# Kernel tuning notes

Measured on AMD Instinct MI355X. Metric: run time of the kernel, lower is better.

The kernel has to match this reference:

```python
import jax, jax.numpy as jnp
import numpy as np

NHEAD = 8
HEAD_DIM = 64
HIDDEN = 512
ROPE_BASE = 10000.0


def _rope_cos_sin(L, dim, dtype):
    inv_freq = 1.0 / (ROPE_BASE ** (jnp.arange(0, dim, 2, dtype=jnp.float32) / dim))
    t = jnp.arange(L, dtype=jnp.float32)
    freqs = jnp.outer(t, inv_freq)                # [L, dim/2]
    emb = jnp.concatenate([freqs, freqs], axis=-1)  # [L, dim]
    return jnp.cos(emb).astype(dtype), jnp.sin(emb).astype(dtype)


def _rotate_half(x):
    x1, x2 = jnp.split(x, 2, axis=-1)
    return jnp.concatenate([-x2, x1], axis=-1)


def setup_inputs() -> dict:
    key = jax.random.key(0)
    ks = jax.random.split(key, 5)
    B, L = 8, 1024
    scale = 0.02
    return {
        "x": jax.random.normal(ks[0], (B, L, HIDDEN), dtype=jnp.float32),
        "Wq": jax.random.normal(ks[1], (HIDDEN, HIDDEN), dtype=jnp.float32) * scale,
        "Wk": jax.random.normal(ks[2], (HIDDEN, HIDDEN), dtype=jnp.float32) * scale,
        "Wv": jax.random.normal(ks[3], (HIDDEN, HIDDEN), dtype=jnp.float32) * scale,
        "Wo": jax.random.normal(ks[4], (HIDDEN, HIDDEN), dtype=jnp.float32) * scale,
    }


def reference(x, Wq, Wk, Wv, Wo):
    B, L, _ = x.shape
    # QKV projections (nn.Linear stores weight as [out, in]; y = x @ W.T)
    def proj(W):
        y = jnp.einsum('bld,ed->ble', x, W)
        return y.reshape(B, L, NHEAD, HEAD_DIM).transpose(0, 2, 1, 3)  # [B,H,L,Dh]
    q, k, v = proj(Wq), proj(Wk), proj(Wv)

    cos, sin = _rope_cos_sin(L, HEAD_DIM, x.dtype)   # [L, Dh]
    cos = cos[None, None]                            # [1,1,L,Dh]
    sin = sin[None, None]
    q = q * cos + _rotate_half(q) * sin
    k = k * cos + _rotate_half(k) * sin

    # scaled dot-product attention (no mask, eval mode -> dropout 0)
    scores = jnp.einsum('bhqd,bhkd->bhqk', q, k) / jnp.sqrt(jnp.asarray(HEAD_DIM, x.dtype))
    attn = jax.nn.softmax(scores, axis=-1)
    out = jnp.einsum('bhqk,bhkd->bhqd', attn, v)     # [B,H,L,Dh]
    out = out.transpose(0, 2, 1, 3).reshape(B, L, HIDDEN)
    return jnp.einsum('ble,oe->blo', out, Wo)
```

## Files before the change

kernel.cpp:

```cpp
#include <hip/hip_runtime.h>
#include <math.h>


#define BB 8
#define LL 1024
#define HH 8
#define DH 64
#define HID 512

typedef __bf16 bf16x8 __attribute__((ext_vector_type(8)));
typedef float f32x4 __attribute__((ext_vector_type(4)));
typedef float f32x16 __attribute__((ext_vector_type(16)));
typedef unsigned short u16x8 __attribute__((ext_vector_type(8)));
typedef unsigned short u16x4 __attribute__((ext_vector_type(4)));
typedef unsigned u32x4 __attribute__((ext_vector_type(4)));

__device__ inline unsigned short f2bf(float f) {
    union { float f; unsigned u; } v; v.f = f;
    unsigned r = v.u + 0x7fffu + ((v.u >> 16) & 1u);
    return (unsigned short)(r >> 16);
}

#define GLOAD_LDS16(g, l) __builtin_amdgcn_global_load_lds( \
    (const __attribute__((address_space(1))) unsigned int*)(g), \
    (__attribute__((address_space(3))) unsigned int*)(l), 16, 0, 0)

__device__ inline bf16x8 pack8(float e0, float e1, float e2, float e3,
                               float e4, float e5, float e6, float e7) {
    unsigned a0, a1, a2, a3;
    asm("v_cvt_pk_bf16_f32 %0, %1, %2" : "=v"(a0) : "v"(e0), "v"(e1));
    asm("v_cvt_pk_bf16_f32 %0, %1, %2" : "=v"(a1) : "v"(e2), "v"(e3));
    asm("v_cvt_pk_bf16_f32 %0, %1, %2" : "=v"(a2) : "v"(e4), "v"(e5));
    asm("v_cvt_pk_bf16_f32 %0, %1, %2" : "=v"(a3) : "v"(e6), "v"(e7));
    asm("v_permlane32_swap_b32 %0, %1" : "+v"(a0), "+v"(a2));
    asm("v_permlane32_swap_b32 %0, %1" : "+v"(a1), "+v"(a3));
    u32x4 wv; wv[0] = a0; wv[1] = a1; wv[2] = a2; wv[3] = a3;
    return *(bf16x8*)&wv;
}

#define Z16 {0.f,0.f,0.f,0.f,0.f,0.f,0.f,0.f,0.f,0.f,0.f,0.f,0.f,0.f,0.f,0.f}

__global__ __launch_bounds__(256) void convert_kernel(
    const float* __restrict__ x, const float* __restrict__ Wq,
    const float* __restrict__ Wk, const float* __restrict__ Wv,
    const float* __restrict__ Wo,
    unsigned short* __restrict__ xb, unsigned short* __restrict__ wqb,
    unsigned short* __restrict__ wkb, unsigned short* __restrict__ wvb,
    unsigned short* __restrict__ wob,
    float* __restrict__ cos_t, float* __restrict__ sin_t)
{
    int blk = blockIdx.x;
    if (blk >= 2560) {
        int idx = (blk - 2560) * 256 + threadIdx.x;
        int l = idx >> 5, j = idx & 31;
        float inv = exp2f(-(float)j * (13.287712379549449f / 32.0f));
        float th = (float)l * inv;
        cos_t[idx] = cosf(th);
        sin_t[idx] = sinf(th);
        return;
    }
    const float* s; unsigned short* d; int off;
    if (blk < 2048) { s = x; d = xb; off = blk; }
    else {
        int t = (blk - 2048) >> 7;
        off = (blk - 2048) & 127;
        s = (t == 0) ? Wq : (t == 1) ? Wk : (t == 2) ? Wv : Wo;
        d = (t == 0) ? wqb : (t == 1) ? wkb : (t == 2) ? wvb : wob;
    }
    size_t base = ((size_t)off * 256 + threadIdx.x) * 8;
    float4 a = *(const float4*)(s + base);
    float4 b = *(const float4*)(s + base + 4);
    u16x8 pk;
    pk[0] = f2bf(a.x); pk[1] = f2bf(a.y); pk[2] = f2bf(a.z); pk[3] = f2bf(a.w);
    pk[4] = f2bf(b.x); pk[5] = f2bf(b.y); pk[6] = f2bf(b.z); pk[7] = f2bf(b.w);
    *(u16x8*)(d + base) = pk;
}

__global__ __launch_bounds__(256) void qkv_gemm_kernel(
    const unsigned short* __restrict__ xb, const unsigned short* __restrict__ Wqb,
    const unsigned short* __restrict__ Wkb, const unsigned short* __restrict__ Wvb,
    const float* __restrict__ cos_t, const float* __restrict__ sin_t,
    unsigned short* __restrict__ Qb, unsigned short* __restrict__ Kb,
    unsigned short* __restrict__ Vt)
{
    __shared__ unsigned short As[128 * 32];
    __shared__ unsigned short Bs[128 * 32];

    const int mt = blockIdx.x;
    const int nt = blockIdx.y;
    const int mbase = mt * 128;
    const int mat = nt >> 2;
    const unsigned short* W = (mat == 0) ? Wqb : ((mat == 1) ? Wkb : Wvb);
    const int nW = (nt & 3) * 128;

    const int tid = threadIdx.x;
    const int w = tid >> 6, lane = tid & 63;
    const int wr = w >> 1, wc = w & 1;
    const int l15 = lane & 15, koff = (lane >> 4) * 8;
    const int srow = (lane >> 2);
    const int scol = (lane & 3) * 8;

    f32x4 acc[4][4];
    #pragma unroll
    for (int i = 0; i < 4; ++i)
        #pragma unroll
        for (int j = 0; j < 4; ++j) acc[i][j] = (f32x4){0.f, 0.f, 0.f, 0.f};

    for (int kc = 0; kc < 512; kc += 32) {
        __syncthreads();
        #pragma unroll
        for (int j = 0; j < 2; ++j) {
            int row = w * 32 + j * 16;
            GLOAD_LDS16(xb + (size_t)(mbase + row + srow) * 512 + kc + scol,
                        As + row * 32);
            GLOAD_LDS16(W + (size_t)(nW + row + srow) * 512 + kc + scol,
                        Bs + row * 32);
        }
        __syncthreads();

        bf16x8 af[4], bf[4];
        #pragma unroll
        for (int mi = 0; mi < 4; ++mi)
            af[mi] = *(const bf16x8*)&As[(wr * 64 + mi * 16 + l15) * 32 + koff];
        #pragma unroll
        for (int ni = 0; ni < 4; ++ni)
            bf[ni] = *(const bf16x8*)&Bs[(wc * 64 + ni * 16 + l15) * 32 + koff];
        #pragma unroll
        for (int mi = 0; mi < 4; ++mi)
            #pragma unroll
            for (int ni = 0; ni < 4; ++ni)
                acc[mi][ni] = __builtin_amdgcn_mfma_f32_16x16x32_bf16(
                    af[mi], bf[ni], acc[mi][ni], 0, 0, 0);
    }

    const int h = (nt & 3) * 2 + wc;
    if (mat < 2) {
        unsigned short* D = (mat == 0) ? Qb : Kb;
        const float sc = (mat == 0) ? 0.18033688011112042f  : 1.0f;
        #pragma unroll
        for (int mi = 0; mi < 4; ++mi) {
            int m = mbase + wr * 64 + mi * 16 + (lane >> 4) * 4;
            int b = m >> 10, l0 = m & 1023;
            #pragma unroll
            for (int r = 0; r < 4; ++r) {
                int l = l0 + r;
                float c0 = cos_t[l * 32 + l15],      s0 = sin_t[l * 32 + l15];
                float c1 = cos_t[l * 32 + 16 + l15], s1 = sin_t[l * 32 + 16 + l15];
                float a0 = acc[mi][0][r], a1 = acc[mi][1][r];
                float a2 = acc[mi][2][r], a3 = acc[mi][3][r];
                float o0 = (a0 * c0 - a2 * s0) * sc;
                float o1 = (a1 * c1 - a3 * s1) * sc;
                float o2 = (a2 * c0 + a0 * s0) * sc;
                float o3 = (a3 * c1 + a1 * s1) * sc;
                size_t rowbase = ((size_t)(b * HH + h) * LL + l) * 64;
                D[rowbase +  0 + l15] = f2bf(o0);
                D[rowbase + 16 + l15] = f2bf(o1);
                D[rowbase + 32 + l15] = f2bf(o2);
                D[rowbase + 48 + l15] = f2bf(o3);
            }
        }
    } else {
        #pragma unroll
        for (int mi = 0; mi < 4; ++mi) {
            int m = mbase + wr * 64 + mi * 16 + (lane >> 4) * 4;
            int b = m >> 10, l0 = m & 1023;
            #pragma unroll
            for (int ni = 0; ni < 4; ++ni) {
                int d = ni * 16 + l15;
                u16x4 pk;
                #pragma unroll
                for (int r = 0; r < 4; ++r) pk[r] = f2bf(acc[mi][ni][r]);
                *(u16x4*)(Vt + ((size_t)(b * HH + h) * 64 + d) * LL + l0) = pk;
            }
        }
    }
}

__global__ __launch_bounds__(256) void attn_kernel(
    const unsigned short* __restrict__ Q, const unsigned short* __restrict__ K,
    const unsigned short* __restrict__ Vt, unsigned short* __restrict__ O)
{
    __shared__ unsigned short Ks[2][64 * 64];
    __shared__ unsigned short Vs[2][64 * 64];

    const int wgid = blockIdx.x;
    const int xcd = wgid & 7;
    const int j = wgid >> 3;
    const int bh = xcd * 8 + (j >> 3);
    const int qt = j & 7;
    const int b = bh >> 3, h = bh & 7;
    const int tid = threadIdx.x;
    const int w = tid >> 6;
    const int lane = tid & 63;
    const int l31 = lane & 31;
    const int hi5 = lane >> 5;

    const unsigned short* Qp = Q + (size_t)bh * LL * 64;
    const unsigned short* Kp = K + (size_t)bh * LL * 64;
    const unsigned short* Vp = Vt + (size_t)bh * 64 * LL;

    const int sr0 = w * 8 + (lane >> 3);
    const int sr1 = 32 + w * 8 + (lane >> 3);
    const int scsw = ((lane & 7) * 8) ^ (((lane >> 3) & 7) * 8);
    const int sd0 = w * 512;
    const int sd1 = 2048 + w * 512;

    const int q0 = qt * 128 + w * 32;

    bf16x8 qf0 = *(const bf16x8*)(Qp + (size_t)(q0 + l31) * 64 +  0 + hi5 * 8);
    bf16x8 qf1 = *(const bf16x8*)(Qp + (size_t)(q0 + l31) * 64 + 16 + hi5 * 8);
    bf16x8 qf2 = *(const bf16x8*)(Qp + (size_t)(q0 + l31) * 64 + 32 + hi5 * 8);
    bf16x8 qf3 = *(const bf16x8*)(Qp + (size_t)(q0 + l31) * 64 + 48 + hi5 * 8);

    const int swz = (l31 & 7) * 8;
    const int co0 = ( 0 + hi5 * 8) ^ swz;
    const int co1 = (16 + hi5 * 8) ^ swz;
    const int co2 = (32 + hi5 * 8) ^ swz;
    const int co3 = (48 + hi5 * 8) ^ swz;
    const int rA = l31 * 64;
    const int rB = (32 + l31) * 64;

    float lsum = 0.f;
    f32x16 opv0 = Z16, opv1 = Z16;

    GLOAD_LDS16(Kp + (size_t)sr0 * 64 + scsw, &Ks[0][sd0]);
    GLOAD_LDS16(Kp + (size_t)sr1 * 64 + scsw, &Ks[0][sd1]);
    GLOAD_LDS16(Vp + (size_t)sr0 * LL + scsw, &Vs[0][sd0]);
    GLOAD_LDS16(Vp + (size_t)sr1 * LL + scsw, &Vs[0][sd1]);
    __syncthreads();

    for (int kt = 0; kt < 16; ++kt) {
        const int cur = kt & 1, nxt = cur ^ 1;
        const int kbase = kt * 64;

        if (kt < 15) {
            GLOAD_LDS16(Kp + (size_t)(kbase + 64 + sr0) * 64 + scsw, &Ks[nxt][sd0]);
            GLOAD_LDS16(Kp + (size_t)(kbase + 64 + sr1) * 64 + scsw, &Ks[nxt][sd1]);
            GLOAD_LDS16(Vp + (size_t)sr0 * LL + kbase + 64 + scsw, &Vs[nxt][sd0]);
            GLOAD_LDS16(Vp + (size_t)sr1 * LL + kbase + 64 + scsw, &Vs[nxt][sd1]);
        }

        f32x16 s0 = Z16, s1 = Z16;
        __builtin_amdgcn_s_setprio(1);
        {
            bf16x8 kA, kB;
            kA = *(const bf16x8*)&Ks[cur][rA + co0];
            kB = *(const bf16x8*)&Ks[cur][rB + co0];
            s0 = __builtin_amdgcn_mfma_f32_32x32x16_bf16(kA, qf0, s0, 0, 0, 0);
            s1 = __builtin_amdgcn_mfma_f32_32x32x16_bf16(kB, qf0, s1, 0, 0, 0);
            kA = *(const bf16x8*)&Ks[cur][rA + co1];
            kB = *(const bf16x8*)&Ks[cur][rB + co1];
            s0 = __builtin_amdgcn_mfma_f32_32x32x16_bf16(kA, qf1, s0, 0, 0, 0);
            s1 = __builtin_amdgcn_mfma_f32_32x32x16_bf16(kB, qf1, s1, 0, 0, 0);
            kA = *(const bf16x8*)&Ks[cur][rA + co2];
            kB = *(const bf16x8*)&Ks[cur][rB + co2];
            s0 = __builtin_amdgcn_mfma_f32_32x32x16_bf16(kA, qf2, s0, 0, 0, 0);
            s1 = __builtin_amdgcn_mfma_f32_32x32x16_bf16(kB, qf2, s1, 0, 0, 0);
            kA = *(const bf16x8*)&Ks[cur][rA + co3];
            kB = *(const bf16x8*)&Ks[cur][rB + co3];
            s0 = __builtin_amdgcn_mfma_f32_32x32x16_bf16(kA, qf3, s0, 0, 0, 0);
            s1 = __builtin_amdgcn_mfma_f32_32x32x16_bf16(kB, qf3, s1, 0, 0, 0);
        }
        __builtin_amdgcn_s_setprio(0);

        float e[16], f[16];
        #pragma unroll
        for (int i = 0; i < 16; ++i) e[i] = exp2f(s0[i]);
        #pragma unroll
        for (int i = 0; i < 16; ++i) f[i] = exp2f(s1[i]);
        lsum += (((e[0]+e[1])+(e[2]+e[3])) + ((e[4]+e[5])+(e[6]+e[7])))
              + (((e[8]+e[9])+(e[10]+e[11])) + ((e[12]+e[13])+(e[14]+e[15])));
        lsum += (((f[0]+f[1])+(f[2]+f[3])) + ((f[4]+f[5])+(f[6]+f[7])))
              + (((f[8]+f[9])+(f[10]+f[11])) + ((f[12]+f[13])+(f[14]+f[15])));
        bf16x8 pf0 = pack8(e[0], e[1], e[2], e[3], e[4], e[5], e[6], e[7]);
        bf16x8 pf1 = pack8(e[8], e[9], e[10], e[11], e[12], e[13], e[14], e[15]);
        bf16x8 pf2 = pack8(f[0], f[1], f[2], f[3], f[4], f[5], f[6], f[7]);
        bf16x8 pf3 = pack8(f[8], f[9], f[10], f[11], f[12], f[13], f[14], f[15]);

        __builtin_amdgcn_s_setprio(1);
        {
            bf16x8 vA, vB;
            vA = *(const bf16x8*)&Vs[cur][rA + co0];
            vB = *(const bf16x8*)&Vs[cur][rB + co0];
            opv0 = __builtin_amdgcn_mfma_f32_32x32x16_bf16(vA, pf0, opv0, 0, 0, 0);
            opv1 = __builtin_amdgcn_mfma_f32_32x32x16_bf16(vB, pf0, opv1, 0, 0, 0);
            vA = *(const bf16x8*)&Vs[cur][rA + co1];
            vB = *(const bf16x8*)&Vs[cur][rB + co1];
            opv0 = __builtin_amdgcn_mfma_f32_32x32x16_bf16(vA, pf1, opv0, 0, 0, 0);
            opv1 = __builtin_amdgcn_mfma_f32_32x32x16_bf16(vB, pf1, opv1, 0, 0, 0);
            vA = *(const bf16x8*)&Vs[cur][rA + co2];
            vB = *(const bf16x8*)&Vs[cur][rB + co2];
            opv0 = __builtin_amdgcn_mfma_f32_32x32x16_bf16(vA, pf2, opv0, 0, 0, 0);
            opv1 = __builtin_amdgcn_mfma_f32_32x32x16_bf16(vB, pf2, opv1, 0, 0, 0);
            vA = *(const bf16x8*)&Vs[cur][rA + co3];
            vB = *(const bf16x8*)&Vs[cur][rB + co3];
            opv0 = __builtin_amdgcn_mfma_f32_32x32x16_bf16(vA, pf3, opv0, 0, 0, 0);
            opv1 = __builtin_amdgcn_mfma_f32_32x32x16_bf16(vB, pf3, opv1, 0, 0, 0);
        }
        __builtin_amdgcn_s_setprio(0);

        __syncthreads();
    }

    lsum += __shfl_xor(lsum, 32);

    const float inv = 1.f / lsum;
    unsigned short* ob = O + (size_t)(b * LL + q0 + l31) * HID + h * 64;
    #pragma unroll
    for (int rg = 0; rg < 4; ++rg) {
        u16x4 pkA, pkB;
        #pragma unroll
        for (int rr = 0; rr < 4; ++rr) {
            pkA[rr] = f2bf(opv0[rg * 4 + rr] * inv);
            pkB[rr] = f2bf(opv1[rg * 4 + rr] * inv);
        }
        *(u16x4*)(ob + rg * 8 + hi5 * 4)      = pkA;
        *(u16x4*)(ob + 32 + rg * 8 + hi5 * 4) = pkB;
    }
}

__global__ __launch_bounds__(256) void out_gemm_kernel(
    const unsigned short* __restrict__ AOb, const unsigned short* __restrict__ Wob,
    float* __restrict__ out)
{
    __shared__ unsigned short As[128 * 32];
    __shared__ unsigned short Bs[64 * 32];

    const int mt = blockIdx.x;
    const int nt = blockIdx.y;
    const int mbase = mt * 128;
    const int nbase = nt * 64;

    const int tid = threadIdx.x;
    const int w = tid >> 6, lane = tid & 63;
    const int wr = w >> 1, wc = w & 1;
    const int l15 = lane & 15, koff = (lane >> 4) * 8;
    const int srow = (lane >> 2);
    const int scol = (lane & 3) * 8;

    f32x4 acc[4][2];
    #pragma unroll
    for (int i = 0; i < 4; ++i)
        #pragma unroll
        for (int j = 0; j < 2; ++j) acc[i][j] = (f32x4){0.f, 0.f, 0.f, 0.f};

    for (int kc = 0; kc < 512; kc += 32) {
        __syncthreads();
        #pragma unroll
        for (int j = 0; j < 2; ++j) {
            int row = w * 32 + j * 16;
            GLOAD_LDS16(AOb + (size_t)(mbase + row + srow) * 512 + kc + scol,
                        As + row * 32);
        }
        {
            int row = w * 16 + srow;
            GLOAD_LDS16(Wob + (size_t)(nbase + row) * 512 + kc + scol,
                        Bs + (w * 16) * 32);
        }
        __syncthreads();

        bf16x8 af[4], bf[2];
        #pragma unroll
        for (int mi = 0; mi < 4; ++mi)
            af[mi] = *(const bf16x8*)&As[(wr * 64 + mi * 16 + l15) * 32 + koff];
        #pragma unroll
        for (int ni = 0; ni < 2; ++ni)
            bf[ni] = *(const bf16x8*)&Bs[(wc * 32 + ni * 16 + l15) * 32 + koff];
        #pragma unroll
        for (int mi = 0; mi < 4; ++mi)
            #pragma unroll
            for (int ni = 0; ni < 2; ++ni)
                acc[mi][ni] = __builtin_amdgcn_mfma_f32_16x16x32_bf16(
                    af[mi], bf[ni], acc[mi][ni], 0, 0, 0);
    }

    #pragma unroll
    for (int mi = 0; mi < 4; ++mi) {
        int m = mbase + wr * 64 + mi * 16 + (lane >> 4) * 4;
        #pragma unroll
        for (int r = 0; r < 4; ++r) {
            size_t rowbase = (size_t)(m + r) * 512 + nbase + wc * 32;
            #pragma unroll
            for (int ni = 0; ni < 2; ++ni)
                out[rowbase + ni * 16 + l15] = acc[mi][ni][r];
        }
    }
}

extern "C" void kernel_launch(void* const* d_in, const int* in_sizes, int n_in,
                              void* d_out, int out_size, void* d_ws, size_t ws_size,
                              hipStream_t stream) {
    const float* x  = (const float*)d_in[0];
    const float* Wq = (const float*)d_in[1];
    const float* Wk = (const float*)d_in[2];
    const float* Wv = (const float*)d_in[3];
    const float* Wo = (const float*)d_in[4];
    float* out = (float*)d_out;

    const size_t tblN = (size_t)LL * 32;
    const size_t qkvN = (size_t)BB * HH * LL * 64;
    const size_t wN   = (size_t)HID * HID;

    float* cos_t = (float*)d_ws;
    float* sin_t = cos_t + tblN;
    unsigned short* Qb  = (unsigned short*)(sin_t + tblN);
    unsigned short* Kb  = Qb + qkvN;
    unsigned short* Vt  = Kb + qkvN;
    unsigned short* xb  = Vt + qkvN;
    unsigned short* Wqb = xb + qkvN;
    unsigned short* Wkb = Wqb + wN;
    unsigned short* Wvb = Wkb + wN;
    unsigned short* Wob = Wvb + wN;
    unsigned short* AOb = Wob + wN;

    hipLaunchKernelGGL(convert_kernel, dim3(2048 + 512 + 128), dim3(256), 0, stream,
                       x, Wq, Wk, Wv, Wo, xb, Wqb, Wkb, Wvb, Wob, cos_t, sin_t);
    hipLaunchKernelGGL(qkv_gemm_kernel, dim3(64, 12), dim3(256), 0, stream,
                       xb, Wqb, Wkb, Wvb, cos_t, sin_t, Qb, Kb, Vt);
    hipLaunchKernelGGL(attn_kernel, dim3(512), dim3(256), 0, stream,
                       Qb, Kb, Vt, AOb);
    hipLaunchKernelGGL(out_gemm_kernel, dim3(64, 8), dim3(256), 0, stream,
                       AOb, Wob, out);
}
```

Measured before the change: 83.64 us.

## Double K-chunk depth in QKV GEMM and attention KV tiles with swizzled LDS

The QKV projection GEMM now stages 64-wide K slices per iteration, with an XOR-swizzled LDS layout to avoid bank conflicts, and issues two MFMAs per tile pair. This halves the number of barrier-synchronised iterations. The attention kernel processes 128 keys per tile instead of 64, so there are half as many barriers and prefetch rounds. This doubles LDS usage per block, which may reduce occupancy, and raises register pressure from more score accumulators and exp values.

```diff
diff --git a/kernel.cpp b/kernel.cpp
--- a/kernel.cpp
+++ b/kernel.cpp
@@ -83,8 +83,8 @@
     unsigned short* __restrict__ Qb, unsigned short* __restrict__ Kb,
     unsigned short* __restrict__ Vt)
 {
-    __shared__ unsigned short As[128 * 32];
-    __shared__ unsigned short Bs[128 * 32];
+    __shared__ unsigned short As[128 * 64];
+    __shared__ unsigned short Bs[128 * 64];
 
     const int mt = blockIdx.x;
     const int nt = blockIdx.y;
@@ -97,8 +97,13 @@
     const int w = tid >> 6, lane = tid & 63;
     const int wr = w >> 1, wc = w & 1;
     const int l15 = lane & 15, koff = (lane >> 4) * 8;
-    const int srow = (lane >> 2);
-    const int scol = (lane & 3) * 8;
+
+    const int srow = w * 8 + (lane >> 3);
+    const int ssw = ((lane & 7) * 8) ^ (((lane >> 3) & 7) * 8);
+
+    const int rsw = (l15 & 7) * 8;
+    const int ck0 = (koff +  0) ^ rsw;
+    const int ck1 = (koff + 32) ^ rsw;
 
     f32x4 acc[4][4];
     #pragma unroll
@@ -106,31 +111,40 @@
         #pragma unroll
         for (int j = 0; j < 4; ++j) acc[i][j] = (f32x4){0.f, 0.f, 0.f, 0.f};
 
-    for (int kc = 0; kc < 512; kc += 32) {
+    for (int kc = 0; kc < 512; kc += 64) {
         __syncthreads();
         #pragma unroll
-        for (int j = 0; j < 2; ++j) {
-            int row = w * 32 + j * 16;
-            GLOAD_LDS16(xb + (size_t)(mbase + row + srow) * 512 + kc + scol,
-                        As + row * 32);
-            GLOAD_LDS16(W + (size_t)(nW + row + srow) * 512 + kc + scol,
-                        Bs + row * 32);
+        for (int j = 0; j < 4; ++j) {
+            int row = j * 32 + srow;
+            GLOAD_LDS16(xb + (size_t)(mbase + row) * 512 + kc + ssw,
+                        As + j * 2048 + w * 512);
+            GLOAD_LDS16(W + (size_t)(nW + row) * 512 + kc + ssw,
+                        Bs + j * 2048 + w * 512);
         }
         __syncthreads();
 
-        bf16x8 af[4], bf[4];
+        bf16x8 af[4][2], bf[4][2];
+        #pragma unroll
+        for (int mi = 0; mi < 4; ++mi) {
+            int r = (wr * 64 + mi * 16 + l15) * 64;
+            af[mi][0] = *(const bf16x8*)&As[r + ck0];
+            af[mi][1] = *(const bf16x8*)&As[r + ck1];
+        }
+        #pragma unroll
+        for (int ni = 0; ni < 4; ++ni) {
+            int r = (wc * 64 + ni * 16 + l15) * 64;
+            bf[ni][0] = *(const bf16x8*)&Bs[r + ck0];
+            bf[ni][1] = *(const bf16x8*)&Bs[r + ck1];
+        }
         #pragma unroll
         for (int mi = 0; mi < 4; ++mi)
-            af[mi] = *(const bf16x8*)&As[(wr * 64 + mi * 16 + l15) * 32 + koff];
-        #pragma unroll
-        for (int ni = 0; ni < 4; ++ni)
-            bf[ni] = *(const bf16x8*)&Bs[(wc * 64 + ni * 16 + l15) * 32 + koff];
-        #pragma unroll
-        for (int mi = 0; mi < 4; ++mi)
-            #pragma unroll
-            for (int ni = 0; ni < 4; ++ni)
+            #pragma unroll
+            for (int ni = 0; ni < 4; ++ni) {
                 acc[mi][ni] = __builtin_amdgcn_mfma_f32_16x16x32_bf16(
-                    af[mi], bf[ni], acc[mi][ni], 0, 0, 0);
+                    af[mi][0], bf[ni][0], acc[mi][ni], 0, 0, 0);
+                acc[mi][ni] = __builtin_amdgcn_mfma_f32_16x16x32_bf16(
+                    af[mi][1], bf[ni][1], acc[mi][ni], 0, 0, 0);
+            }
     }
 
     const int h = (nt & 3) * 2 + wc;
@@ -180,8 +194,8 @@
     const unsigned short* __restrict__ Q, const unsigned short* __restrict__ K,
     const unsigned short* __restrict__ Vt, unsigned short* __restrict__ O)
 {
-    __shared__ unsigned short Ks[2][64 * 64];
-    __shared__ unsigned short Vs[2][64 * 64];
+    __shared__ unsigned short Ks[2][128 * 64];
+    __shared__ unsigned short Vs[2][64 * 128];
 
     const int wgid = blockIdx.x;
     const int xcd = wgid & 7;
@@ -199,11 +213,10 @@
     const unsigned short* Kp = K + (size_t)bh * LL * 64;
     const unsigned short* Vp = Vt + (size_t)bh * 64 * LL;
 
-    const int sr0 = w * 8 + (lane >> 3);
-    const int sr1 = 32 + w * 8 + (lane >> 3);
-    const int scsw = ((lane & 7) * 8) ^ (((lane >> 3) & 7) * 8);
-    const int sd0 = w * 512;
-    const int sd1 = 2048 + w * 512;
+    const int srK = w * 8 + (lane >> 3);
+    const int sswK = ((lane & 7) * 8) ^ (((lane >> 3) & 7) * 8);
+    const int srV = w * 4 + (lane >> 4);
+    const int sswV = ((lane & 15) * 8) ^ ((srV & 7) * 8);
 
     const int q0 = qt * 128 + w * 32;
 
@@ -217,85 +230,136 @@
     const int co1 = (16 + hi5 * 8) ^ swz;
     const int co2 = (32 + hi5 * 8) ^ swz;
     const int co3 = (48 + hi5 * 8) ^ swz;
-    const int rA = l31 * 64;
-    const int rB = (32 + l31) * 64;
+    const int rK = l31 * 64;
+    int cv[8];
+    #pragma unroll
+    for (int ksl = 0; ksl < 8; ++ksl) cv[ksl] = (ksl * 16 + hi5 * 8) ^ swz;
+    const int rVA = l31 * 128;
+    const int rVB = rVA + 32 * 128;
 
     float lsum = 0.f;
     f32x16 opv0 = Z16, opv1 = Z16;
 
-    GLOAD_LDS16(Kp + (size_t)sr0 * 64 + scsw, &Ks[0][sd0]);
-    GLOAD_LDS16(Kp + (size_t)sr1 * 64 + scsw, &Ks[0][sd1]);
-    GLOAD_LDS16(Vp + (size_t)sr0 * LL + scsw, &Vs[0][sd0]);
-    GLOAD_LDS16(Vp + (size_t)sr1 * LL + scsw, &Vs[0][sd1]);
+    #pragma unroll
+    for (int c = 0; c < 4; ++c) {
+        GLOAD_LDS16(Kp + (size_t)(c * 32 + srK) * 64 + sswK, &Ks[0][c * 2048 + w * 512]);
+        GLOAD_LDS16(Vp + (size_t)(c * 16 + srV) * LL + sswV, &Vs[0][c * 2048 + w * 512]);
+    }
     __syncthreads();
 
-    for (int kt = 0; kt < 16; ++kt) {
+    for (int kt = 0; kt < 8; ++kt) {
         const int cur = kt & 1, nxt = cur ^ 1;
-        const int kbase = kt * 64;
-
-        if (kt < 15) {
-            GLOAD_LDS16(Kp + (size_t)(kbase + 64 + sr0) * 64 + scsw, &Ks[nxt][sd0]);
-            GLOAD_LDS16(Kp + (size_t)(kbase + 64 + sr1) * 64 + scsw, &Ks[nxt][sd1]);
-            GLOAD_LDS16(Vp + (size_t)sr0 * LL + kbase + 64 + scsw, &Vs[nxt][sd0]);
-            GLOAD_LDS16(Vp + (size_t)sr1 * LL + kbase + 64 + scsw, &Vs[nxt][sd1]);
-        }
-
-        f32x16 s0 = Z16, s1 = Z16;
+        const int kbase = kt * 128;
+
+        if (kt < 7) {
+            #pragma unroll
+            for (int c = 0; c < 4; ++c) {
+                GLOAD_LDS16(Kp + (size_t)(kbase + 128 + c * 32 + srK) * 64 + sswK,
+                            &Ks[nxt][c * 2048 + w * 512]);
+                GLOAD_LDS16(Vp + (size_t)(c * 16 + srV) * LL + kbase + 128 + sswV,
+                            &Vs[nxt][c * 2048 + w * 512]);
+            }
+        }
+
+        f32x16 s0 = Z16, s1 = Z16, s2 = Z16, s3 = Z16;
         __builtin_amdgcn_s_setprio(1);
         {
-            bf16x8 kA, kB;
-            kA = *(const bf16x8*)&Ks[cur][rA + co0];
-            kB = *(const bf16x8*)&Ks[cur][rB + co0];
+            bf16x8 kA;
+            kA = *(const bf16x8*)&Ks[cur][0 * 2048 + rK + co0];
             s0 = __builtin_amdgcn_mfma_f32_32x32x16_bf16(kA, qf0, s0, 0, 0, 0);
-            s1 = __builtin_amdgcn_mfma_f32_32x32x16_bf16(kB, qf0, s1, 0, 0, 0);
-            kA = *(const bf16x8*)&Ks[cur][rA + co1];
-            kB = *(const bf16x8*)&Ks[cur][rB + co1];
+            kA = *(const bf16x8*)&Ks[cur][0 * 2048 + rK + co1];
             s0 = __builtin_amdgcn_mfma_f32_32x32x16_bf16(kA, qf1, s0, 0, 0, 0);
-            s1 = __builtin_amdgcn_mfma_f32_32x32x16_bf16(kB, qf1, s1, 0, 0, 0);
-            kA = *(const bf16x8*)&Ks[cur][rA + co2];
-            kB = *(const bf16x8*)&Ks[cur][rB + co2];
+            kA = *(const bf16x8*)&Ks[cur][0 * 2048 + rK + co2];
             s0 = __builtin_amdgcn_mfma_f32_32x32x16_bf16(kA, qf2, s0, 0, 0, 0);
-            s1 = __builtin_amdgcn_mfma_f32_32x32x16_bf16(kB, qf2, s1, 0, 0, 0);
-            kA = *(const bf16x8*)&Ks[cur][rA + co3];
-            kB = *(const bf16x8*)&Ks[cur][rB + co3];
+            kA = *(const bf16x8*)&Ks[cur][0 * 2048 + rK + co3];
             s0 = __builtin_amdgcn_mfma_f32_32x32x16_bf16(kA, qf3, s0, 0, 0, 0);
-            s1 = __builtin_amdgcn_mfma_f32_32x32x16_bf16(kB, qf3, s1, 0, 0, 0);
+
+            kA = *(const bf16x8*)&Ks[cur][1 * 2048 + rK + co0];
+            s1 = __builtin_amdgcn_mfma_f32_32x32x16_bf16(kA, qf0, s1, 0, 0, 0);
+            kA = *(const bf16x8*)&Ks[cur][1 * 2048 + rK + co1];
+            s1 = __builtin_amdgcn_mfma_f32_32x32x16_bf16(kA, qf1, s1, 0, 0, 0);
+            kA = *(const bf16x8*)&Ks[cur][1 * 2048 + rK + co2];
+            s1 = __builtin_amdgcn_mfma_f32_32x32x16_bf16(kA, qf2, s1, 0, 0, 0);
+            kA = *(const bf16x8*)&Ks[cur][1 * 2048 + rK + co3];
+            s1 = __builtin_amdgcn_mfma_f32_32x32x16_bf16(kA, qf3, s1, 0, 0, 0);
+
+            kA = *(const bf16x8*)&Ks[cur][2 * 2048 + rK + co0];
+            s2 = __builtin_amdgcn_mfma_f32_32x32x16_bf16(kA, qf0, s2, 0, 0, 0);
+            kA = *(const bf16x8*)&Ks[cur][2 * 2048 + rK + co1];
+            s2 = __builtin_amdgcn_mfma_f32_32x32x16_bf16(kA, qf1, s2, 0, 0, 0);
+            kA = *(const bf16x8*)&Ks[cur][2 * 2048 + rK + co2];
+            s2 = __builtin_amdgcn_mfma_f32_32x32x16_bf16(kA, qf2, s2, 0, 0, 0);
+            kA = *(const bf16x8*)&Ks[cur][2 * 2048 + rK + co3];
+            s2 = __builtin_amdgcn_mfma_f32_32x32x16_bf16(kA, qf3, s2, 0, 0, 0);
+
+            kA = *(const bf16x8*)&Ks[cur][3 * 2048 + rK + co0];
+            s3 = __builtin_amdgcn_mfma_f32_32x32x16_bf16(kA, qf0, s3, 0, 0, 0);
+            kA = *(const bf16x8*)&Ks[cur][3 * 2048 + rK + co1];
+            s3 = __builtin_amdgcn_mfma_f32_32x32x16_bf16(kA, qf1, s3, 0, 0, 0);
+            kA = *(const bf16x8*)&Ks[cur][3 * 2048 + rK + co2];
+            s3 = __builtin_amdgcn_mfma_f32_32x32x16_bf16(kA, qf2, s3, 0, 0, 0);
+            kA = *(const bf16x8*)&Ks[cur][3 * 2048 + rK + co3];
+            s3 = __builtin_amdgcn_mfma_f32_32x32x16_bf16(kA, qf3, s3, 0, 0, 0);
         }
         __builtin_amdgcn_s_setprio(0);
 
-        float e[16], f[16];
-        #pragma unroll
-        for (int i = 0; i < 16; ++i) e[i] = exp2f(s0[i]);
-        #pragma unroll
-        for (int i = 0; i < 16; ++i) f[i] = exp2f(s1[i]);
-        lsum += (((e[0]+e[1])+(e[2]+e[3])) + ((e[4]+e[5])+(e[6]+e[7])))
-              + (((e[8]+e[9])+(e[10]+e[11])) + ((e[12]+e[13])+(e[14]+e[15])));
-        lsum += (((f[0]+f[1])+(f[2]+f[3])) + ((f[4]+f[5])+(f[6]+f[7])))
-              + (((f[8]+f[9])+(f[10]+f[11])) + ((f[12]+f[13])+(f[14]+f[15])));
+        float e[16], f[16], g[16], hh[16];
+        #pragma unroll
+        for (int i = 0; i < 16; ++i) e[i]  = exp2f(s0[i]);
+        #pragma unroll
+        for (int i = 0; i < 16; ++i) f[i]  = exp2f(s1[i]);
+        #pragma unroll
+        for (int i = 0; i < 16; ++i) g[i]  = exp2f(s2[i]);
+        #pragma unroll
+        for (int i = 0; i < 16; ++i) hh[i] = exp2f(s3[i]);
+        #pragma unroll
+        for (int i = 0; i < 16; ++i) lsum += e[i] + f[i];
+        #pragma unroll
+        for (int i = 0; i < 16; ++i) lsum += g[i] + hh[i];
         bf16x8 pf0 = pack8(e[0], e[1], e[2], e[3], e[4], e[5], e[6], e[7]);
         bf16x8 pf1 = pack8(e[8], e[9], e[10], e[11], e[12], e[13], e[14], e[15]);
         bf16x8 pf2 = pack8(f[0], f[1], f[2], f[3], f[4], f[5], f[6], f[7]);
         bf16x8 pf3 = pack8(f[8], f[9], f[10], f[11], f[12], f[13], f[14], f[15]);
+        bf16x8 pf4 = pack8(g[0], g[1], g[2], g[3], g[4], g[5], g[6], g[7]);
+        bf16x8 pf5 = pack8(g[8], g[9], g[10], g[11], g[12], g[13], g[14], g[15]);
+        bf16x8 pf6 = pack8(hh[0], hh[1], hh[2], hh[3], hh[4], hh[5], hh[6], hh[7]);
+        bf16x8 pf7 = pack8(hh[8], hh[9], hh[10], hh[11], hh[12], hh[13], hh[14], hh[15]);
 
         __builtin_amdgcn_s_setprio(1);
         {
             bf16x8 vA, vB;
-            vA = *(const bf16x8*)&Vs[cur][rA + co0];
-            vB = *(const bf16x8*)&Vs[cur][rB + co0];
+            vA = *(const bf16x8*)&Vs[cur][rVA + cv[0]];
+            vB = *(const bf16x8*)&Vs[cur][rVB + cv[0]];
             opv0 = __builtin_amdgcn_mfma_f32_32x32x16_bf16(vA, pf0, opv0, 0, 0, 0);
             opv1 = __builtin_amdgcn_mfma_f32_32x32x16_bf16(vB, pf0, opv1, 0, 0, 0);
-            vA = *(const bf16x8*)&Vs[cur][rA + co1];
-            vB = *(const bf16x8*)&Vs[cur][rB + co1];
+            vA = *(const bf16x8*)&Vs[cur][rVA + cv[1]];
+            vB = *(const bf16x8*)&Vs[cur][rVB + cv[1]];
             opv0 = __builtin_amdgcn_mfma_f32_32x32x16_bf16(vA, pf1, opv0, 0, 0, 0);
             opv1 = __builtin_amdgcn_mfma_f32_32x32x16_bf16(vB, pf1, opv1, 0, 0, 0);
-            vA = *(const bf16x8*)&Vs[cur][rA + co2];
-            vB = *(const bf16x8*)&Vs[cur][rB + co2];
+            vA = *(const bf16x8*)&Vs[cur][rVA + cv[2]];
+            vB = *(const bf16x8*)&Vs[cur][rVB + cv[2]];
             opv0 = __builtin_amdgcn_mfma_f32_32x32x16_bf16(vA, pf2, opv0, 0, 0, 0);
             opv1 = __builtin_amdgcn_mfma_f32_32x32x16_bf16(vB, pf2, opv1, 0, 0, 0);
-            vA = *(const bf16x8*)&Vs[cur][rA + co3];
-            vB = *(const bf16x8*)&Vs[cur][rB + co3];
+            vA = *(const bf16x8*)&Vs[cur][rVA + cv[3]];
+            vB = *(const bf16x8*)&Vs[cur][rVB + cv[3]];
             opv0 = __builtin_amdgcn_mfma_f32_32x32x16_bf16(vA, pf3, opv0, 0, 0, 0);
             opv1 = __builtin_amdgcn_mfma_f32_32x32x16_bf16(vB, pf3, opv1, 0, 0, 0);
+            vA = *(const bf16x8*)&Vs[cur][rVA + cv[4]];
+            vB = *(const bf16x8*)&Vs[cur][rVB + cv[4]];
+            opv0 = __builtin_amdgcn_mfma_f32_32x32x16_bf16(vA, pf4, opv0, 0, 0, 0);
+            opv1 = __builtin_amdgcn_mfma_f32_32x32x16_bf16(vB, pf4, opv1, 0, 0, 0);
+            vA = *(const bf16x8*)&Vs[cur][rVA + cv[5]];
+            vB = *(const bf16x8*)&Vs[cur][rVB + cv[5]];
+            opv0 = __builtin_amdgcn_mfma_f32_32x32x16_bf16(vA, pf5, opv0, 0, 0, 0);
+            opv1 = __builtin_amdgcn_mfma_f32_32x32x16_bf16(vB, pf5, opv1, 0, 0, 0);
+            vA = *(const bf16x8*)&Vs[cur][rVA + cv[6]];
+            vB = *(const bf16x8*)&Vs[cur][rVB + cv[6]];
+            opv0 = __builtin_amdgcn_mfma_f32_32x32x16_bf16(vA, pf6, opv0, 0, 0, 0);
+            opv1 = __builtin_amdgcn_mfma_f32_32x32x16_bf16(vB, pf6, opv1, 0, 0, 0);
+            vA = *(const bf16x8*)&Vs[cur][rVA + cv[7]];
+            vB = *(const bf16x8*)&Vs[cur][rVB + cv[7]];
+            opv0 = __builtin_amdgcn_mfma_f32_32x32x16_bf16(vA, pf7, opv0, 0, 0, 0);
+            opv1 = __builtin_amdgcn_mfma_f32_32x32x16_bf16(vB, pf7, opv1, 0, 0, 0);
         }
         __builtin_amdgcn_s_setprio(0);
 
```

Measured after the change: 92.17 us. 10.2% more time.

## Deepen QKV GEMM k-tile to 64 with XOR-swizzled LDS; refine attention barriers

Applied to the files above, without the earlier changes.

The QKV projection GEMM now stages 64-wide K chunks instead of 32, which halves the number of loop iterations and barriers. The LDS layout uses an XOR swizzle on column offsets to avoid bank conflicts when the 16-lane fragments are read back. In the attention kernel, the full __syncthreads at loop top and bottom is replaced by explicit vmcnt waits plus raw s_barrier. This lets the prefetch of the next K/V tile stay in flight while the current tile is consumed. The trade-off is double the LDS per block in the GEMM, and fragile hand-counted waitcnt values.

```diff
diff --git a/kernel.cpp b/kernel.cpp
--- a/kernel.cpp
+++ b/kernel.cpp
@@ -83,8 +83,8 @@
     unsigned short* __restrict__ Qb, unsigned short* __restrict__ Kb,
     unsigned short* __restrict__ Vt)
 {
-    __shared__ unsigned short As[128 * 32];
-    __shared__ unsigned short Bs[128 * 32];
+    __shared__ unsigned short As[128 * 64];
+    __shared__ unsigned short Bs[128 * 64];
 
     const int mt = blockIdx.x;
     const int nt = blockIdx.y;
@@ -97,8 +97,13 @@
     const int w = tid >> 6, lane = tid & 63;
     const int wr = w >> 1, wc = w & 1;
     const int l15 = lane & 15, koff = (lane >> 4) * 8;
-    const int srow = (lane >> 2);
-    const int scol = (lane & 3) * 8;
+
+    const int srow = w * 8 + (lane >> 3);
+    const int ssw = ((lane & 7) * 8) ^ (((lane >> 3) & 7) * 8);
+
+    const int rsw = (l15 & 7) * 8;
+    const int ck0 = (koff +  0) ^ rsw;
+    const int ck1 = (koff + 32) ^ rsw;
 
     f32x4 acc[4][4];
     #pragma unroll
@@ -106,31 +111,40 @@
         #pragma unroll
         for (int j = 0; j < 4; ++j) acc[i][j] = (f32x4){0.f, 0.f, 0.f, 0.f};
 
-    for (int kc = 0; kc < 512; kc += 32) {
+    for (int kc = 0; kc < 512; kc += 64) {
         __syncthreads();
         #pragma unroll
-        for (int j = 0; j < 2; ++j) {
-            int row = w * 32 + j * 16;
-            GLOAD_LDS16(xb + (size_t)(mbase + row + srow) * 512 + kc + scol,
-                        As + row * 32);
-            GLOAD_LDS16(W + (size_t)(nW + row + srow) * 512 + kc + scol,
-                        Bs + row * 32);
+        for (int j = 0; j < 4; ++j) {
+            int row = j * 32 + srow;
+            GLOAD_LDS16(xb + (size_t)(mbase + row) * 512 + kc + ssw,
+                        As + j * 2048 + w * 512);
+            GLOAD_LDS16(W + (size_t)(nW + row) * 512 + kc + ssw,
+                        Bs + j * 2048 + w * 512);
         }
         __syncthreads();
 
-        bf16x8 af[4], bf[4];
-        #pragma unroll
-        for (int mi = 0; mi < 4; ++mi)
-            af[mi] = *(const bf16x8*)&As[(wr * 64 + mi * 16 + l15) * 32 + koff];
-        #pragma unroll
-        for (int ni = 0; ni < 4; ++ni)
-            bf[ni] = *(const bf16x8*)&Bs[(wc * 64 + ni * 16 + l15) * 32 + koff];
+        bf16x8 af[4][2], bf[4][2];
+        #pragma unroll
+        for (int mi = 0; mi < 4; ++mi) {
+            int r = (wr * 64 + mi * 16 + l15) * 64;
+            af[mi][0] = *(const bf16x8*)&As[r + ck0];
+            af[mi][1] = *(const bf16x8*)&As[r + ck1];
+        }
+        #pragma unroll
+        for (int ni = 0; ni < 4; ++ni) {
+            int r = (wc * 64 + ni * 16 + l15) * 64;
+            bf[ni][0] = *(const bf16x8*)&Bs[r + ck0];
+            bf[ni][1] = *(const bf16x8*)&Bs[r + ck1];
+        }
         #pragma unroll
         for (int mi = 0; mi < 4; ++mi)
             #pragma unroll
-            for (int ni = 0; ni < 4; ++ni)
+            for (int ni = 0; ni < 4; ++ni) {
                 acc[mi][ni] = __builtin_amdgcn_mfma_f32_16x16x32_bf16(
-                    af[mi], bf[ni], acc[mi][ni], 0, 0, 0);
+                    af[mi][0], bf[ni][0], acc[mi][ni], 0, 0, 0);
+                acc[mi][ni] = __builtin_amdgcn_mfma_f32_16x16x32_bf16(
+                    af[mi][1], bf[ni][1], acc[mi][ni], 0, 0, 0);
+            }
     }
 
     const int h = (nt & 3) * 2 + wc;
@@ -238,7 +252,11 @@
             GLOAD_LDS16(Kp + (size_t)(kbase + 64 + sr1) * 64 + scsw, &Ks[nxt][sd1]);
             GLOAD_LDS16(Vp + (size_t)sr0 * LL + kbase + 64 + scsw, &Vs[nxt][sd0]);
             GLOAD_LDS16(Vp + (size_t)sr1 * LL + kbase + 64 + scsw, &Vs[nxt][sd1]);
-        }
+            asm volatile("s_waitcnt vmcnt(4)" ::: "memory");
+        } else {
+            asm volatile("s_waitcnt vmcnt(0)" ::: "memory");
+        }
+        __builtin_amdgcn_s_barrier();
 
         f32x16 s0 = Z16, s1 = Z16;
         __builtin_amdgcn_s_setprio(1);
@@ -299,7 +317,8 @@
         }
         __builtin_amdgcn_s_setprio(0);
 
-        __syncthreads();
+        asm volatile("" ::: "memory");
+        __builtin_amdgcn_s_barrier();
     }
 
     lsum += __shfl_xor(lsum, 32);
```

After: 81.88 us. -2.1%, faster.

## Double-buffer GEMM LDS tiles with swizzle, fine-grained waits, and raw exp2

Applied to the files above, without the earlier changes.

Both projection GEMMs now double-buffer their LDS tiles, prefetching the next K-chunk while MFMAs run on the current one. They wait on vmcnt counts plus raw s_barrier instead of full __syncthreads, and use an XOR swizzle on the LDS column to cut bank conflicts. The attention loop gets the same partial vmcnt wait and barrier treatment, unroll 2, and swaps exp2f for the raw v_exp_f32 instruction. This doubles LDS use per block and relies on hand-counted vmcnt values being correct.

```diff
diff --git a/kernel.cpp b/kernel.cpp
--- a/kernel.cpp
+++ b/kernel.cpp
@@ -19,6 +19,12 @@
     union { float f; unsigned u; } v; v.f = f;
     unsigned r = v.u + 0x7fffu + ((v.u >> 16) & 1u);
     return (unsigned short)(r >> 16);
+}
+
+__device__ inline float fexp2(float x) {
+    float r;
+    asm("v_exp_f32 %0, %1" : "=v"(r) : "v"(x));
+    return r;
 }
 
 #define GLOAD_LDS16(g, l) __builtin_amdgcn_global_load_lds( \
@@ -83,8 +89,8 @@
     unsigned short* __restrict__ Qb, unsigned short* __restrict__ Kb,
     unsigned short* __restrict__ Vt)
 {
-    __shared__ unsigned short As[128 * 32];
-    __shared__ unsigned short Bs[128 * 32];
+    __shared__ unsigned short As[2][128 * 32];
+    __shared__ unsigned short Bs[2][128 * 32];
 
     const int mt = blockIdx.x;
     const int nt = blockIdx.y;
@@ -97,8 +103,11 @@
     const int w = tid >> 6, lane = tid & 63;
     const int wr = w >> 1, wc = w & 1;
     const int l15 = lane & 15, koff = (lane >> 4) * 8;
-    const int srow = (lane >> 2);
-    const int scol = (lane & 3) * 8;
+
+    const int srow = lane >> 2;
+    const int ssw = ((lane & 3) * 8) ^ ((srow & 3) * 8);
+
+    const int ck = koff ^ ((l15 & 3) * 8);
 
     f32x4 acc[4][4];
     #pragma unroll
@@ -106,31 +115,51 @@
         #pragma unroll
         for (int j = 0; j < 4; ++j) acc[i][j] = (f32x4){0.f, 0.f, 0.f, 0.f};
 
-    for (int kc = 0; kc < 512; kc += 32) {
-        __syncthreads();
-        #pragma unroll
-        for (int j = 0; j < 2; ++j) {
-            int row = w * 32 + j * 16;
-            GLOAD_LDS16(xb + (size_t)(mbase + row + srow) * 512 + kc + scol,
-                        As + row * 32);
-            GLOAD_LDS16(W + (size_t)(nW + row + srow) * 512 + kc + scol,
-                        Bs + row * 32);
-        }
-        __syncthreads();
+    #pragma unroll
+    for (int j = 0; j < 2; ++j) {
+        int row = w * 32 + j * 16;
+        GLOAD_LDS16(xb + (size_t)(mbase + row + srow) * 512 + ssw, As[0] + row * 32);
+        GLOAD_LDS16(W  + (size_t)(nW   + row + srow) * 512 + ssw, Bs[0] + row * 32);
+    }
+    __syncthreads();
+
+    #pragma unroll 2
+    for (int s = 0; s < 16; ++s) {
+        const int cur = s & 1, nxt = cur ^ 1;
+        const int kn = s * 32 + 32;
+        if (s < 15) {
+            #pragma unroll
+            for (int j = 0; j < 2; ++j) {
+                int row = w * 32 + j * 16;
+                GLOAD_LDS16(xb + (size_t)(mbase + row + srow) * 512 + kn + ssw,
+                            As[nxt] + row * 32);
+                GLOAD_LDS16(W  + (size_t)(nW   + row + srow) * 512 + kn + ssw,
+                            Bs[nxt] + row * 32);
+            }
+            asm volatile("s_waitcnt vmcnt(4)" ::: "memory");
+        } else {
+            asm volatile("s_waitcnt vmcnt(0)" ::: "memory");
+        }
+        __builtin_amdgcn_s_barrier();
 
         bf16x8 af[4], bf[4];
         #pragma unroll
         for (int mi = 0; mi < 4; ++mi)
-            af[mi] = *(const bf16x8*)&As[(wr * 64 + mi * 16 + l15) * 32 + koff];
+            af[mi] = *(const bf16x8*)&As[cur][(wr * 64 + mi * 16 + l15) * 32 + ck];
         #pragma unroll
         for (int ni = 0; ni < 4; ++ni)
-            bf[ni] = *(const bf16x8*)&Bs[(wc * 64 + ni * 16 + l15) * 32 + koff];
+            bf[ni] = *(const bf16x8*)&Bs[cur][(wc * 64 + ni * 16 + l15) * 32 + ck];
+        __builtin_amdgcn_s_setprio(1);
         #pragma unroll
         for (int mi = 0; mi < 4; ++mi)
             #pragma unroll
             for (int ni = 0; ni < 4; ++ni)
                 acc[mi][ni] = __builtin_amdgcn_mfma_f32_16x16x32_bf16(
                     af[mi], bf[ni], acc[mi][ni], 0, 0, 0);
+        __builtin_amdgcn_s_setprio(0);
+
+        asm volatile("" ::: "memory");
+        __builtin_amdgcn_s_barrier();
     }
 
     const int h = (nt & 3) * 2 + wc;
@@ -229,6 +258,7 @@
     GLOAD_LDS16(Vp + (size_t)sr1 * LL + scsw, &Vs[0][sd1]);
     __syncthreads();
 
+    #pragma unroll 2
     for (int kt = 0; kt < 16; ++kt) {
         const int cur = kt & 1, nxt = cur ^ 1;
         const int kbase = kt * 64;
@@ -238,7 +268,11 @@
             GLOAD_LDS16(Kp + (size_t)(kbase + 64 + sr1) * 64 + scsw, &Ks[nxt][sd1]);
             GLOAD_LDS16(Vp + (size_t)sr0 * LL + kbase + 64 + scsw, &Vs[nxt][sd0]);
             GLOAD_LDS16(Vp + (size_t)sr1 * LL + kbase + 64 + scsw, &Vs[nxt][sd1]);
-        }
+            asm volatile("s_waitcnt vmcnt(4)" ::: "memory");
+        } else {
+            asm volatile("s_waitcnt vmcnt(0)" ::: "memory");
+        }
+        __builtin_amdgcn_s_barrier();
 
         f32x16 s0 = Z16, s1 = Z16;
         __builtin_amdgcn_s_setprio(1);
@@ -265,9 +299,9 @@
 
         float e[16], f[16];
         #pragma unroll
-        for (int i = 0; i < 16; ++i) e[i] = exp2f(s0[i]);
-        #pragma unroll
-        for (int i = 0; i < 16; ++i) f[i] = exp2f(s1[i]);
+        for (int i = 0; i < 16; ++i) e[i] = fexp2(s0[i]);
+        #pragma unroll
+        for (int i = 0; i < 16; ++i) f[i] = fexp2(s1[i]);
         lsum += (((e[0]+e[1])+(e[2]+e[3])) + ((e[4]+e[5])+(e[6]+e[7])))
               + (((e[8]+e[9])+(e[10]+e[11])) + ((e[12]+e[13])+(e[14]+e[15])));
         lsum += (((f[0]+f[1])+(f[2]+f[3])) + ((f[4]+f[5])+(f[6]+f[7])))
@@ -299,7 +333,8 @@
         }
         __builtin_amdgcn_s_setprio(0);
 
-        __syncthreads();
+        asm volatile("" ::: "memory");
+        __builtin_amdgcn_s_barrier();
     }
 
     lsum += __shfl_xor(lsum, 32);
@@ -323,8 +358,8 @@
     const unsigned short* __restrict__ AOb, const unsigned short* __restrict__ Wob,
     float* __restrict__ out)
 {
-    __shared__ unsigned short As[128 * 32];
-    __shared__ unsigned short Bs[64 * 32];
+    __shared__ unsigned short As[2][128 * 32];
+    __shared__ unsigned short Bs[2][64 * 32];
 
     const int mt = blockIdx.x;
     const int nt = blockIdx.y;
@@ -335,8 +370,10 @@
     const int w = tid >> 6, lane = tid & 63;
     const int wr = w >> 1, wc = w & 1;
     const int l15 = lane & 15, koff = (lane >> 4) * 8;
-    const int srow = (lane >> 2);
-    const int scol = (lane & 3) * 8;
+
+    const int srow = lane >> 2;
+    const int ssw = ((lane & 3) * 8) ^ ((srow & 3) * 8);
+    const int ck = koff ^ ((l15 & 3) * 8);
 
     f32x4 acc[4][2];
     #pragma unroll
@@ -344,34 +381,51 @@
         #pragma unroll
         for (int j = 0; j < 2; ++j) acc[i][j] = (f32x4){0.f, 0.f, 0.f, 0.f};
 
-    for (int kc = 0; kc < 512; kc += 32) {
-        __syncthreads();
-        #pragma unroll
-        for (int j = 0; j < 2; ++j) {
-            int row = w * 32 + j * 16;
-            GLOAD_LDS16(AOb + (size_t)(mbase + row + srow) * 512 + kc + scol,
-                        As + row * 32);
-        }
-        {
-            int row = w * 16 + srow;
-            GLOAD_LDS16(Wob + (size_t)(nbase + row) * 512 + kc + scol,
-                        Bs + (w * 16) * 32);
-        }
-        __syncthreads();
+    #pragma unroll
+    for (int j = 0; j < 2; ++j) {
+        int row = w * 32 + j * 16;
+        GLOAD_LDS16(AOb + (size_t)(mbase + row + srow) * 512 + ssw, As[0] + row * 32);
+    }
+    GLOAD_LDS16(Wob + (size_t)(nbase + w * 16 + srow) * 512 + ssw, Bs[0] + (w * 16) * 32);
+    __syncthreads();
+
+    #pragma unroll 2
+    for (int s = 0; s < 16; ++s) {
+        const int cur = s & 1, nxt = cur ^ 1;
+        const int kn = s * 32 + 32;
+        if (s < 15) {
+            #pragma unroll
+            for (int j = 0; j < 2; ++j) {
+                int row = w * 32 + j * 16;
+                GLOAD_LDS16(AOb + (size_t)(mbase + row + srow) * 512 + kn + ssw,
+                            As[nxt] + row * 32);
+            }
+            GLOAD_LDS16(Wob + (size_t)(nbase + w * 16 + srow) * 512 + kn + ssw,
+                        Bs[nxt] + (w * 16) * 32);
+            asm volatile("s_waitcnt vmcnt(3)" ::: "memory");
+        } else {
+            asm volatile("s_waitcnt vmcnt(0)" ::: "memory");
+        }
+        __builtin_amdgcn_s_barrier();
 
         bf16x8 af[4], bf[2];
         #pragma unroll
         for (int mi = 0; mi < 4; ++mi)
-            af[mi] = *(const bf16x8*)&As[(wr * 64 + mi * 16 + l15) * 32 + koff];
+            af[mi] = *(const bf16x8*)&As[cur][(wr * 64 + mi * 16 + l15) * 32 + ck];
         #pragma unroll
         for (int ni = 0; ni < 2; ++ni)
-            bf[ni] = *(const bf16x8*)&Bs[(wc * 32 + ni * 16 + l15) * 32 + koff];
+            bf[ni] = *(const bf16x8*)&Bs[cur][(wc * 32 + ni * 16 + l15) * 32 + ck];
+        __builtin_amdgcn_s_setprio(1);
         #pragma unroll
         for (int mi = 0; mi < 4; ++mi)
             #pragma unroll
             for (int ni = 0; ni < 2; ++ni)
                 acc[mi][ni] = __builtin_amdgcn_mfma_f32_16x16x32_bf16(
                     af[mi], bf[ni], acc[mi][ni], 0, 0, 0);
+        __builtin_amdgcn_s_setprio(0);
+
+        asm volatile("" ::: "memory");
+        __builtin_amdgcn_s_barrier();
     }
 
     #pragma unroll
```

Result: faster. 77.16 us (-7.8%).
